# Kernel tuning notes

Hardware: AMD Instinct MI355X
Metric: run time of the kernel (lower is better)

## Reference

```python
import jax, jax.numpy as jnp
import numpy as np

N = 16383        # complete binary tree, 14 levels
D_NODE = 512
D_SSM = 512
D_STATE = 16
MAX_DEPTH = 14   # number of BFS levels (depth 0..13)
LN_EPS = 1e-5


def setup_inputs() -> dict:
    key = jax.random.key(0)
    ks = jax.random.split(key, 8)
    # tree structure: parent[i] = (i-1)//2, root has parent -1; BFS order == index order
    parent = np.concatenate([np.array([-1]), (np.arange(1, N) - 1) // 2]).astype(np.int64)
    depth = np.floor(np.log2(np.arange(N) + 1)).astype(np.int32)
    s = jax.random.normal(ks[0], (N, D_NODE), jnp.float32)
    w = jax.random.uniform(ks[1], (N,), jnp.float32, minval=0.01, maxval=1.0)
    # parameters (xavier-ish scales)
    W_in = jax.random.normal(ks[2], (D_SSM, D_NODE + 1), jnp.float32) * (1.0 / np.sqrt(D_NODE + 1))
    b_in = jnp.zeros((D_SSM,), jnp.float32)
    W_delta = jax.random.normal(ks[3], (D_SSM, D_SSM), jnp.float32) * (1.0 / np.sqrt(D_SSM))
    # dt-style bias init: softplus(b) ~ dt in [1e-3, 1e-1]
    dt = jnp.exp(jax.random.uniform(ks[4], (D_SSM,), jnp.float32) * (np.log(0.1) - np.log(0.001)) + np.log(0.001))
    b_delta = dt + jnp.log(-jnp.expm1(-dt))
    W_w = jax.random.normal(ks[5], (D_SSM, 1), jnp.float32)
    b_w = jnp.zeros((D_SSM,), jnp.float32)
    A_log = jnp.log(jnp.broadcast_to(jnp.arange(1.0, D_STATE + 1.0, dtype=jnp.float32)[None, :], (D_SSM, D_STATE)))
    D = jnp.ones((D_SSM,), jnp.float32)
    W_B = jax.random.normal(ks[6], (D_STATE, D_SSM), jnp.float32) * (1.0 / np.sqrt(D_SSM))
    b_B = jnp.zeros((D_STATE,), jnp.float32)
    W_C = jax.random.normal(ks[7], (D_STATE, D_SSM), jnp.float32) * (1.0 / np.sqrt(D_SSM))
    b_C = jnp.zeros((D_STATE,), jnp.float32)
    gamma = jnp.ones((D_SSM,), jnp.float32)
    beta = jnp.zeros((D_SSM,), jnp.float32)
    return {"s": s, "w": w, "parent": jnp.asarray(parent), "depth": jnp.asarray(depth),
            "W_in": W_in, "b_in": b_in, "W_delta": W_delta, "b_delta": b_delta,
            "W_w": W_w, "b_w": b_w, "A_log": A_log, "D": D,
            "W_B": W_B, "b_B": b_B, "W_C": W_C, "b_C": b_C,
            "gamma": gamma, "beta": beta}


def reference(s, w, parent, depth, W_in, b_in, W_delta, b_delta, W_w, b_w,
              A_log, D, W_B, b_B, W_C, b_C, gamma, beta):
    n = s.shape[0]
    log_w = jnp.log(w + 1e-6)[:, None]                       # [N, 1]
    feat = jnp.concatenate([s, log_w], axis=1)               # [N, d_node+1]
    x = feat @ W_in.T + b_in                                 # [N, d_ssm]
    delta = jax.nn.softplus(x @ W_delta.T + b_delta) * jax.nn.sigmoid(log_w @ W_w.T + b_w)  # [N, d_ssm]
    A = -jnp.exp(A_log)                                      # [d_ssm, d_state]
    B = x @ W_B.T + b_B                                      # [N, d_state]
    C = x @ W_C.T + b_C                                      # [N, d_state]
    A_bar = jnp.exp(delta[:, :, None] * A[None])             # [N, d_ssm, d_state]
    Bx = (delta * x)[:, :, None] * B[:, None, :]             # [N, d_ssm, d_state]
    # level-parallel tree scan: all nodes at BFS depth l updated together
    par = jnp.maximum(parent, 0)
    has_par = (parent >= 0)[:, None, None]
    H = jnp.zeros((n, A_bar.shape[1], A_bar.shape[2]), x.dtype)
    for lvl in range(MAX_DEPTH):
        h_par = jnp.where(has_par, jnp.take(H, par, axis=0), 0.0)
        H = jnp.where((depth == lvl)[:, None, None], A_bar * h_par + Bx, H)
    Y = jnp.einsum('nds,ns->nd', H, C) + D * x               # [N, d_ssm]
    mu = jnp.mean(Y, axis=-1, keepdims=True)
    var = jnp.var(Y, axis=-1, keepdims=True)
    return (Y - mu) / jnp.sqrt(var + LN_EPS) * gamma + beta
```

## Files before the change

kernel.cpp:

```cpp
#include <hip/hip_runtime.h>
#include <hip/hip_bf16.h>
#include <math.h>

#define D_SSM 512
#define D_STATE 16
#define CKPT_BASE 511
#define N_CKPT 512
#define MPAD 16384

typedef __attribute__((ext_vector_type(8))) short short8;
typedef __attribute__((ext_vector_type(4))) float floatx4;

__device__ __forceinline__ unsigned short f2bf(float f) {
    unsigned int u = __float_as_uint(f);
    unsigned int r = (u + 0x7fffu + ((u >> 16) & 1u)) >> 16;
    return (unsigned short)r;
}
__device__ __forceinline__ float bf2f(unsigned short u) {
    return __uint_as_float(((unsigned int)u) << 16);
}
__device__ __forceinline__ void g2lds16(const void* g, void* l) {
    __builtin_amdgcn_global_load_lds(
        (const __attribute__((address_space(1))) void*)g,
        (__attribute__((address_space(3))) void*)l, 16, 0, 0);
}

__device__ __forceinline__ void pw_powers(float r, float* p) {
    float r2 = r * r, r4 = r2 * r2, r8 = r4 * r4;
    p[0] = r;          p[1] = r2;         p[2] = r2 * r;     p[3] = r4;
    p[4] = r4 * r;     p[5] = r4 * r2;    p[6] = r4 * p[2];  p[7] = r8;
    p[8] = r8 * r;     p[9] = r8 * r2;    p[10] = r8 * p[2]; p[11] = r8 * r4;
    p[12] = r8 * p[4]; p[13] = r8 * p[5]; p[14] = r8 * p[6]; p[15] = r8 * r8;
}

__global__ __launch_bounds__(256) void prep_kernel(
    const float* __restrict__ s, const float* __restrict__ w,
    const float* __restrict__ W_in, const float* __restrict__ W_delta,
    const float* __restrict__ W_B, const float* __restrict__ W_C,
    unsigned short* __restrict__ s_bf, float* __restrict__ lw,
    unsigned short* __restrict__ Win_bf, unsigned short* __restrict__ Wd_bf,
    int Nn)
{
    const int b = blockIdx.x, t = threadIdx.x;
    if (b < MPAD) {
        unsigned int pack = 0;
        if (b < Nn) {
            float2 sv = *(const float2*)(s + (size_t)b * 512 + t * 2);
            pack = (unsigned int)f2bf(sv.x) | ((unsigned int)f2bf(sv.y) << 16);
        }
        *(unsigned int*)(s_bf + (size_t)b * 512 + t * 2) = pack;
        if (t == 0) lw[b] = (b < Nn) ? logf(w[b] + 1e-6f) : 0.f;
    } else if (b < MPAD + 512) {
        int c = b - MPAD;
        float a0 = W_in[(size_t)c * 513 + t * 2];
        float a1 = W_in[(size_t)c * 513 + t * 2 + 1];
        *(unsigned int*)(Win_bf + (size_t)c * 512 + t * 2) =
            (unsigned int)f2bf(a0) | ((unsigned int)f2bf(a1) << 16);
    } else if (b < MPAD + 1024) {
        int c = b - MPAD - 512;
        float2 wv = *(const float2*)(W_delta + (size_t)c * 512 + t * 2);
        *(unsigned int*)(Wd_bf + (size_t)c * 512 + t * 2) =
            (unsigned int)f2bf(wv.x) | ((unsigned int)f2bf(wv.y) << 16);
    } else {
        int c = b - MPAD - 1024;
        float2 wv; wv.x = 0.f; wv.y = 0.f;
        if (c < 16)      wv = *(const float2*)(W_B + (size_t)c * 512 + t * 2);
        else if (c < 32) wv = *(const float2*)(W_C + (size_t)(c - 16) * 512 + t * 2);
        *(unsigned int*)(Wd_bf + (size_t)(512 + c) * 512 + t * 2) =
            (unsigned int)f2bf(wv.x) | ((unsigned int)f2bf(wv.y) << 16);
    }
}

__global__ __launch_bounds__(256) void gemm_mfma(
    const unsigned short* __restrict__ Abf,
    const unsigned short* __restrict__ Wbf,
    float* __restrict__ outf,
    unsigned short* __restrict__ outbf,
    const float* __restrict__ bias,
    const float* __restrict__ lw,
    const float* __restrict__ wcol, int wcol_stride,
    const float* __restrict__ bw,
    const float* __restrict__ b_B, const float* __restrict__ b_C,
    float* __restrict__ Bm, float* __restrict__ Cm,
    int mode)
{
    __shared__ __align__(16) short As[2][128 * 32];
    __shared__ __align__(16) short Bs[2][128 * 32];
    const int tid = threadIdx.x;
    const int wave = tid >> 6, lane = tid & 63;

    const int nwg  = gridDim.x * gridDim.y;
    const int orig = blockIdx.y * gridDim.x + blockIdx.x;
    const int wsw  = (orig & 7) * (nwg >> 3) + (orig >> 3);
    const int bx   = wsw % gridDim.x;
    const int by   = wsw / gridDim.x;
    const int row0 = by * 128;
    const int col0 = bx * 128;

    const int wr = (wave >> 1) * 64;
    const int wc = (wave & 1) * 64;

    floatx4 acc[4][4] = {};

    const int srow = lane >> 2;
    const int sg   = (lane & 3) ^ ((srow >> 1) & 3);
    const int scol = sg * 8;

    const unsigned short* Ag = Abf + (size_t)(row0 + wave * 16 + srow) * 512 + scol;
    const unsigned short* Wg = Wbf + (size_t)(col0 + wave * 16 + srow) * 512 + scol;
    char* Al = (char*)&As[0][0] + wave * 1024;
    char* Bl = (char*)&Bs[0][0] + wave * 1024;

    #define STAGE(buf, k0)                                              \
        do {                                                            \
            g2lds16(Ag + (k0),            Al + (buf) * 8192);           \
            g2lds16(Ag + 64 * 512 + (k0), Al + (buf) * 8192 + 4096);    \
            g2lds16(Wg + (k0),            Bl + (buf) * 8192);           \
            g2lds16(Wg + 64 * 512 + (k0), Bl + (buf) * 8192 + 4096);    \
        } while (0)

    STAGE(0, 0);
    __syncthreads();

    for (int it = 0; it < 16; ++it) {
        const int cur = it & 1;
        if (it < 15) STAGE(cur ^ 1, (it + 1) * 32);

        short8 af[4], bfr[4];
        #pragma unroll
        for (int i = 0; i < 4; i++) {
            int m = wr + i * 16 + (lane & 15);
            int gm = (lane >> 4) ^ ((m >> 1) & 3);
            af[i] = *(const short8*)&As[cur][m * 32 + gm * 8];
        }
        #pragma unroll
        for (int j = 0; j < 4; j++) {
            int n = wc + j * 16 + (lane & 15);
            int gn = (lane >> 4) ^ ((n >> 1) & 3);
            bfr[j] = *(const short8*)&Bs[cur][n * 32 + gn * 8];
        }
        #pragma unroll
        for (int i = 0; i < 4; i++)
            #pragma unroll
            for (int j = 0; j < 4; j++)
                acc[i][j] = __builtin_amdgcn_mfma_f32_16x16x32_bf16(af[i], bfr[j], acc[i][j], 0, 0, 0);
        __syncthreads();
    }
    #undef STAGE

    if (col0 >= 512) {
        #pragma unroll
        for (int i = 0; i < 4; i++) {
            #pragma unroll
            for (int reg = 0; reg < 4; reg++) {
                int r = row0 + wr + i * 16 + (lane >> 4) * 4 + reg;
                #pragma unroll
                for (int j = 0; j < 4; j++) {
                    int c2 = wc + j * 16 + (lane & 15);
                    float z = acc[i][j][reg];
                    if (c2 < 16)      Bm[(size_t)r * 16 + c2]        = z + b_B[c2];
                    else if (c2 < 32) Cm[(size_t)r * 16 + (c2 - 16)] = z + b_C[c2 - 16];
                }
            }
        }
        return;
    }

    #pragma unroll
    for (int i = 0; i < 4; i++) {
        #pragma unroll
        for (int reg = 0; reg < 4; reg++) {
            int r = row0 + wr + i * 16 + (lane >> 4) * 4 + reg;
            float lwr = lw[r];
            #pragma unroll
            for (int j = 0; j < 4; j++) {
                int c = col0 + wc + j * 16 + (lane & 15);
                float z = acc[i][j][reg] + bias[c];
                if (mode == 0) {
                    float o = z + lwr * wcol[(size_t)c * wcol_stride];
                    outbf[(size_t)r * 512 + c] = f2bf(o);
                } else {
                    float sp = (z > 15.f) ? z : __logf(1.f + __expf(z));
                    float sg2 = __builtin_amdgcn_rcpf(1.f + __expf(-(lwr * wcol[c] + bw[c])));
                    outf[(size_t)r * 512 + c] = sp * sg2;
                }
            }
        }
    }
}

__global__ __launch_bounds__(512) void scan_shallow(
    const unsigned short* __restrict__ x_bf, const float* __restrict__ delta,
    const float* __restrict__ Bm, const float* __restrict__ Cm,
    const float* __restrict__ A_log, const float* __restrict__ Dv,
    const float* __restrict__ gamma, const float* __restrict__ beta,
    float* __restrict__ out)
{
    __shared__ __align__(16) float Banc[9][16];
    __shared__ __align__(16) float Cn[16];
    __shared__ float red[16];
    const int n = blockIdx.x;
    const int d = threadIdx.x;

    if (d < 144) {
        int k = d >> 4, s = d & 15;
        int a = n;
        for (int q = 0; q < 9; q++) if (q < k) a = (a < 0) ? -1 : ((a - 1) >> 1);
        Banc[k][s] = (a >= 0) ? Bm[(size_t)a * 16 + s] : 0.f;
    }
    if (d >= 240 && d < 256) Cn[d - 240] = Cm[(size_t)n * 16 + (d - 240)];
    __syncthreads();

    float As0 = -__expf(A_log[d * 16]);
    bool fast = true;
    #pragma unroll
    for (int s = 1; s < 16; s++) {
        float As = -__expf(A_log[d * 16 + s]);
        fast = fast && (fabsf(As - (float)(s + 1) * As0) <= 1e-4f * (float)(s + 1));
    }

    float acc[16];
    #pragma unroll
    for (int s = 0; s < 16; s++) acc[s] = 0.f;

    float cum = 0.f;
    int a = n;
    #pragma unroll
    for (int k = 0; k < 9; k++) {
        if (a >= 0) {
            float da = delta[(size_t)a * 512 + d];
            float bx = da * bf2f(x_bf[(size_t)a * 512 + d]);
            if (fast) {
                float r = __expf(As0 * cum);
                float pw[16]; pw_powers(r, pw);
                const floatx4* B4 = (const floatx4*)&Banc[k][0];
                #pragma unroll
                for (int q = 0; q < 4; q++) {
                    floatx4 b = B4[q];
                    #pragma unroll
                    for (int u = 0; u < 4; u++) {
                        int s = q * 4 + u;
                        acc[s] = fmaf(bx * pw[s], b[u], acc[s]);
                    }
                }
            } else {
                #pragma unroll
                for (int s = 0; s < 16; s++) {
                    float As = -__expf(A_log[d * 16 + s]);
                    acc[s] = fmaf(bx * __expf(As * cum), Banc[k][s], acc[s]);
                }
            }
            cum += da;
            a = (a - 1) >> 1;
        }
    }

    float xv = bf2f(x_bf[(size_t)n * 512 + d]);
    float y0 = 0.f, y1 = 0.f;
    const floatx4* C4 = (const floatx4*)&Cn[0];
    #pragma unroll
    for (int q = 0; q < 4; q++) {
        floatx4 c = C4[q];
        #pragma unroll
        for (int u = 0; u < 4; u++) {
            int s = q * 4 + u;
            if (s & 1) y1 = fmaf(c[u], acc[s], y1);
            else       y0 = fmaf(c[u], acc[s], y0);
        }
    }
    float y = fmaf(Dv[d], xv, y0 + y1);

    float s1 = y, s2 = y * y;
    #pragma unroll
    for (int off = 32; off > 0; off >>= 1) {
        s1 += __shfl_xor(s1, off);
        s2 += __shfl_xor(s2, off);
    }
    int wid = d >> 6, lane = d & 63;
    if (lane == 0) { red[wid] = s1; red[wid + 8] = s2; }
    __syncthreads();
    float S1 = 0.f, S2 = 0.f;
    #pragma unroll
    for (int k = 0; k < 8; k++) { S1 += red[k]; S2 += red[k + 8]; }
    float mu = S1 * (1.f / 512.f);
    float var = S2 * (1.f / 512.f) - mu * mu;
    float inv = rsqrtf(var + 1e-5f);
    out[(size_t)n * 512 + d] = (y - mu) * inv * gamma[d] + beta[d];
}

__global__ __launch_bounds__(512) void scan_deep(
    const unsigned short* __restrict__ x_bf, const float* __restrict__ delta,
    const float* __restrict__ Bm, const float* __restrict__ Cm,
    const float* __restrict__ A_log, const float* __restrict__ Dv,
    const float* __restrict__ gamma, const float* __restrict__ beta,
    float* __restrict__ out)
{
    __shared__ float Y[16][512];
    __shared__ __align__(16) float BCs[31][32];
    __shared__ __align__(16) float Banc[10][16];
    __shared__ int nid[16];
    const int p = blockIdx.x;
    const int d = threadIdx.x;
    const int a9 = CKPT_BASE + p;

    for (int idx = d; idx < 31 * 32; idx += 512) {
        int i = idx >> 5, c = idx & 31;
        int v = i + 1;
        int j = 31 - __builtin_clz((unsigned)v);
        int node = ((a9 + 1) << j) - 1 + (v - (1 << j));
        BCs[i][c] = (c < 16) ? Bm[(size_t)node * 16 + c] : Cm[(size_t)node * 16 + (c - 16)];
    }
    if (d < 160) {
        int k = d >> 4, s = d & 15;
        int a = a9;
        for (int q = 0; q < k; q++) a = (a - 1) >> 1;
        Banc[k][s] = Bm[(size_t)a * 16 + s];
    }
    __syncthreads();

    float As0 = -__expf(A_log[d * 16]);
    bool fast = true;
    #pragma unroll
    for (int s = 1; s < 16; s++) {
        float As = -__expf(A_log[d * 16 + s]);
        fast = fast && (fabsf(As - (float)(s + 1) * As0) <= 1e-4f * (float)(s + 1));
    }
    const float dvd = Dv[d];

    float H9v[16];
    #pragma unroll
    for (int s = 0; s < 16; s++) H9v[s] = 0.f;
    {
        float cum = 0.f;
        int a = a9;
        #pragma unroll
        for (int k = 0; k < 10; k++) {
            float da = delta[(size_t)a * 512 + d];
            float bx = da * bf2f(x_bf[(size_t)a * 512 + d]);
            if (fast) {
                float r = __expf(As0 * cum);
                float pw[16]; pw_powers(r, pw);
                const floatx4* B4 = (const floatx4*)&Banc[k][0];
                #pragma unroll
                for (int q = 0; q < 4; q++) {
                    floatx4 b = B4[q];
                    #pragma unroll
                    for (int u = 0; u < 4; u++) {
                        int s = q * 4 + u;
                        H9v[s] = fmaf(bx * pw[s], b[u], H9v[s]);
                    }
                }
            } else {
                #pragma unroll
                for (int s = 0; s < 16; s++) {
                    float As = -__expf(A_log[d * 16 + s]);
                    H9v[s] = fmaf(bx * __expf(As * cum), Banc[k][s], H9v[s]);
                }
            }
            cum += da;
            a = (a - 1) >> 1;
        }
    }

    auto step = [&](int n, int bfs, const float* Hp, float* Hc, int slot) {
        float dlt = delta[(size_t)n * 512 + d];
        float xv = bf2f(x_bf[(size_t)n * 512 + d]);
        float bx = dlt * xv;
        const floatx4* B4 = (const floatx4*)&BCs[bfs][0];
        const floatx4* C4 = (const floatx4*)&BCs[bfs][16];
        float y0 = 0.f, y1 = 0.f;
        if (fast) {
            float r = __expf(As0 * dlt);
            float pw[16]; pw_powers(r, pw);
            #pragma unroll
            for (int q = 0; q < 4; q++) {
                floatx4 b = B4[q], c = C4[q];
                #pragma unroll
                for (int u = 0; u < 4; u++) {
                    int s = q * 4 + u;
                    Hc[s] = fmaf(pw[s], Hp[s], bx * b[u]);
                    if (s & 1) y1 = fmaf(c[u], Hc[s], y1);
                    else       y0 = fmaf(c[u], Hc[s], y0);
                }
            }
        } else {
            #pragma unroll
            for (int s = 0; s < 16; s++) {
                float Ab = __expf(dlt * (-__expf(A_log[d * 16 + s])));
                Hc[s] = fmaf(Ab, Hp[s], bx * BCs[bfs][s]);
                float cc = BCs[bfs][16 + s];
                if (s & 1) y1 = fmaf(cc, Hc[s], y1);
                else       y0 = fmaf(cc, Hc[s], y0);
            }
        }
        Y[slot][d] = fmaf(dvd, xv, y0 + y1);
        if (d == 0) nid[slot] = n;
    };

    auto flush = [&](int cnt) {
        const int w = d >> 6, lane = d & 63;
        for (int i = w; i < cnt; i += 8) {
            int n = nid[i];
            float v[8]; float s1 = 0.f, s2 = 0.f;
            #pragma unroll
            for (int k = 0; k < 8; k++) {
                v[k] = Y[i][lane + 64 * k];
                s1 += v[k]; s2 += v[k] * v[k];
            }
            #pragma unroll
            for (int off = 32; off > 0; off >>= 1) {
                s1 += __shfl_xor(s1, off);
                s2 += __shfl_xor(s2, off);
            }
            float mu = s1 * (1.f / 512.f);
            float inv = rsqrtf(s2 * (1.f / 512.f) - mu * mu + 1e-5f);
            #pragma unroll
            for (int k = 0; k < 8; k++) {
                int ch = lane + 64 * k;
                out[(size_t)n * 512 + ch] = (v[k] - mu) * inv * gamma[ch] + beta[ch];
            }
        }
    };

    float H10[16], H11[16], H12[16], H13[16];
    #pragma unroll
    for (int c0 = 0; c0 < 2; c0++) {
        int slot = 0;
        if (c0 == 0) {
            float xv = bf2f(x_bf[(size_t)a9 * 512 + d]);
            const floatx4* C4 = (const floatx4*)&BCs[0][16];
            float y0 = 0.f, y1 = 0.f;
            #pragma unroll
            for (int q = 0; q < 4; q++) {
                floatx4 c = C4[q];
                #pragma unroll
                for (int u = 0; u < 4; u++) {
                    int s = q * 4 + u;
                    if (s & 1) y1 = fmaf(c[u], H9v[s], y1);
                    else       y0 = fmaf(c[u], H9v[s], y0);
                }
            }
            Y[0][d] = fmaf(dvd, xv, y0 + y1);
            if (d == 0) nid[0] = a9;
            slot = 1;
        }
        int n10 = 2 * a9 + 1 + c0;
        step(n10, 1 + c0, H9v, H10, slot++);
        #pragma unroll
        for (int c1 = 0; c1 < 2; c1++) {
            int n11 = 2 * n10 + 1 + c1;
            step(n11, 3 + 2 * c0 + c1, H10, H11, slot++);
            #pragma unroll
            for (int c2 = 0; c2 < 2; c2++) {
                int n12 = 2 * n11 + 1 + c2;
                step(n12, 7 + 4 * c0 + 2 * c1 + c2, H11, H12, slot++);
                #pragma unroll
                for (int c3 = 0; c3 < 2; c3++) {
                    int n13 = 2 * n12 + 1 + c3;
                    step(n13, 15 + 8 * c0 + 4 * c1 + 2 * c2 + c3, H12, H13, slot++);
                }
            }
        }
        __syncthreads();
        flush(c0 == 0 ? 16 : 15);
        __syncthreads();
    }
}

extern "C" void kernel_launch(void* const* d_in, const int* in_sizes, int n_in,
                              void* d_out, int out_size, void* d_ws, size_t ws_size,
                              hipStream_t stream) {
    const float* s_in   = (const float*)d_in[0];
    const float* w      = (const float*)d_in[1];
    const float* W_in    = (const float*)d_in[4];
    const float* b_in    = (const float*)d_in[5];
    const float* W_delta = (const float*)d_in[6];
    const float* b_delta = (const float*)d_in[7];
    const float* W_w     = (const float*)d_in[8];
    const float* b_w     = (const float*)d_in[9];
    const float* A_log   = (const float*)d_in[10];
    const float* Dv      = (const float*)d_in[11];
    const float* W_B     = (const float*)d_in[12];
    const float* b_B     = (const float*)d_in[13];
    const float* W_C     = (const float*)d_in[14];
    const float* b_C     = (const float*)d_in[15];
    const float* gamma   = (const float*)d_in[16];
    const float* beta    = (const float*)d_in[17];
    float* out = (float*)d_out;

    const int Nn = in_sizes[1];

    float* ws    = (float*)d_ws;
    float* lw    = ws;
    float* delta = lw + MPAD;
    float* Bm    = delta + (size_t)MPAD * 512;
    float* Cm    = Bm + (size_t)MPAD * 16;
    unsigned short* s_bf  = (unsigned short*)(Cm + (size_t)MPAD * 16);
    unsigned short* x_bf  = s_bf + (size_t)MPAD * 512;
    unsigned short* Win_bf = x_bf + (size_t)MPAD * 512;
    unsigned short* Wd_bf  = Win_bf + 512 * 512;

    prep_kernel<<<MPAD + 1024 + 128, 256, 0, stream>>>(s_in, w, W_in, W_delta, W_B, W_C,
                                                       s_bf, lw, Win_bf, Wd_bf, Nn);

    dim3 g1(4, 128);
    gemm_mfma<<<g1, 256, 0, stream>>>(s_bf, Win_bf, nullptr, x_bf,
                                      b_in, lw, W_in + 512, 513, nullptr,
                                      nullptr, nullptr, nullptr, nullptr, 0);
    dim3 g2(5, 128);
    gemm_mfma<<<g2, 256, 0, stream>>>(x_bf, Wd_bf, delta, nullptr,
                                      b_delta, lw, W_w, 1, b_w,
                                      b_B, b_C, Bm, Cm, 1);

    scan_shallow<<<CKPT_BASE, 512, 0, stream>>>(x_bf, delta, Bm, Cm, A_log, Dv,
                                                gamma, beta, out);

    scan_deep<<<N_CKPT, 512, 0, stream>>>(x_bf, delta, Bm, Cm, A_log, Dv,
                                          gamma, beta, out);
}
```

Baseline: 222.2 us.

## Fuse shallow and deep scan kernels with prefetching and precomputed A tables

Merges the shallow-node and deep-subtree scan kernels into one launch. Deep blocks take the first block indices and shallow blocks fill in behind them. The per-channel A_log exp and fast-path check move into the prep kernel as small tables. The deep path now software-prefetches ancestor and subtree delta/x values into registers ahead of use, and leaf nodes skip storing state. This removes a launch and hides global-load latency, at the cost of more registers, with launch bounds set to 4 blocks per CU.

Result: slower. 234.1 us (+5.3%).

```diff
diff --git a/kernel.cpp b/kernel.cpp
--- a/kernel.cpp
+++ b/kernel.cpp
@@ -37,8 +37,10 @@
     const float* __restrict__ s, const float* __restrict__ w,
     const float* __restrict__ W_in, const float* __restrict__ W_delta,
     const float* __restrict__ W_B, const float* __restrict__ W_C,
+    const float* __restrict__ A_log,
     unsigned short* __restrict__ s_bf, float* __restrict__ lw,
     unsigned short* __restrict__ Win_bf, unsigned short* __restrict__ Wd_bf,
+    float* __restrict__ As_tab, int* __restrict__ fast_tab,
     int Nn)
 {
     const int b = blockIdx.x, t = threadIdx.x;
@@ -61,13 +63,24 @@
         float2 wv = *(const float2*)(W_delta + (size_t)c * 512 + t * 2);
         *(unsigned int*)(Wd_bf + (size_t)c * 512 + t * 2) =
             (unsigned int)f2bf(wv.x) | ((unsigned int)f2bf(wv.y) << 16);
-    } else {
+    } else if (b < MPAD + 1024 + 128) {
         int c = b - MPAD - 1024;
         float2 wv; wv.x = 0.f; wv.y = 0.f;
         if (c < 16)      wv = *(const float2*)(W_B + (size_t)c * 512 + t * 2);
         else if (c < 32) wv = *(const float2*)(W_C + (size_t)(c - 16) * 512 + t * 2);
         *(unsigned int*)(Wd_bf + (size_t)(512 + c) * 512 + t * 2) =
             (unsigned int)f2bf(wv.x) | ((unsigned int)f2bf(wv.y) << 16);
+    } else {
+        int ch = (b - (MPAD + 1024 + 128)) * 256 + t;
+        float As0 = -__expf(A_log[ch * 16]);
+        bool ok = true;
+        #pragma unroll
+        for (int q = 1; q < 16; q++) {
+            float As = -__expf(A_log[ch * 16 + q]);
+            ok = ok && (fabsf(As - (float)(q + 1) * As0) <= 1e-4f * (float)(q + 1));
+        }
+        As_tab[ch] = As0;
+        fast_tab[ch] = ok ? 1 : 0;
     }
 }
 
@@ -189,281 +202,351 @@
     }
 }
 
-__global__ __launch_bounds__(512) void scan_shallow(
+__global__ __launch_bounds__(512, 4) void scan_fused(
     const unsigned short* __restrict__ x_bf, const float* __restrict__ delta,
     const float* __restrict__ Bm, const float* __restrict__ Cm,
     const float* __restrict__ A_log, const float* __restrict__ Dv,
     const float* __restrict__ gamma, const float* __restrict__ beta,
+    const float* __restrict__ As_tab, const int* __restrict__ fast_tab,
     float* __restrict__ out)
 {
-    __shared__ __align__(16) float Banc[9][16];
-    __shared__ __align__(16) float Cn[16];
-    __shared__ float red[16];
-    const int n = blockIdx.x;
+    __shared__ __align__(16) float SMEM[16 * 512 + 31 * 32 + 10 * 16];
+    __shared__ int nid[16];
+    const int bid = blockIdx.x;
     const int d = threadIdx.x;
 
-    if (d < 144) {
-        int k = d >> 4, s = d & 15;
-        int a = n;
-        for (int q = 0; q < 9; q++) if (q < k) a = (a < 0) ? -1 : ((a - 1) >> 1);
-        Banc[k][s] = (a >= 0) ? Bm[(size_t)a * 16 + s] : 0.f;
-    }
-    if (d >= 240 && d < 256) Cn[d - 240] = Cm[(size_t)n * 16 + (d - 240)];
-    __syncthreads();
-
-    float As0 = -__expf(A_log[d * 16]);
-    bool fast = true;
-    #pragma unroll
-    for (int s = 1; s < 16; s++) {
-        float As = -__expf(A_log[d * 16 + s]);
-        fast = fast && (fabsf(As - (float)(s + 1) * As0) <= 1e-4f * (float)(s + 1));
-    }
-
-    float acc[16];
-    #pragma unroll
-    for (int s = 0; s < 16; s++) acc[s] = 0.f;
-
-    float cum = 0.f;
-    int a = n;
-    #pragma unroll
-    for (int k = 0; k < 9; k++) {
-        if (a >= 0) {
-            float da = delta[(size_t)a * 512 + d];
-            float bx = da * bf2f(x_bf[(size_t)a * 512 + d]);
+    const float As0 = As_tab[d];
+    const bool fast = fast_tab[d] != 0;
+    const float dvd = Dv[d];
+
+    if (bid < N_CKPT) {
+        const int a9 = CKPT_BASE + bid;
+        float* const Yb   = SMEM;
+        float* const BCs  = SMEM + 8192;
+        float* const Banc = SMEM + 8192 + 992;
+
+        for (int idx = d; idx < 31 * 32; idx += 512) {
+            int i = idx >> 5, c = idx & 31;
+            int v = i + 1;
+            int j = 31 - __builtin_clz((unsigned)v);
+            int node = ((a9 + 1) << j) - 1 + (v - (1 << j));
+            BCs[i * 32 + c] = (c < 16) ? Bm[(size_t)node * 16 + c]
+                                       : Cm[(size_t)node * 16 + (c - 16)];
+        }
+        if (d < 160) {
+            int k = d >> 4, ss = d & 15;
+            int a = a9;
+            for (int q = 0; q < k; q++) a = (a - 1) >> 1;
+            Banc[k * 16 + ss] = Bm[(size_t)a * 16 + ss];
+        }
+
+        float adl[10]; unsigned short axr[10];
+        {
+            int a = a9;
+            #pragma unroll
+            for (int k = 0; k < 10; k++) {
+                adl[k] = delta[(size_t)a * 512 + d];
+                axr[k] = x_bf[(size_t)a * 512 + d];
+                a = (a - 1) >> 1;
+            }
+        }
+
+        const int n10a = 2 * a9 + 1, n10b = 2 * a9 + 2;
+        float pdl[2][7]; unsigned short pxr[2][7]; int pid[2][7];
+        auto pf7 = [&](int n11, float* dl, unsigned short* xr, int* id) {
+            id[0] = n11;          id[1] = 2 * n11 + 1; id[2] = 2 * id[1] + 1;
+            id[3] = id[2] + 1;    id[4] = 2 * n11 + 2; id[5] = 2 * id[4] + 1;
+            id[6] = id[5] + 1;
+            #pragma unroll
+            for (int q = 0; q < 7; q++) {
+                dl[q] = delta[(size_t)id[q] * 512 + d];
+                xr[q] = x_bf[(size_t)id[q] * 512 + d];
+            }
+        };
+        float d10a = delta[(size_t)n10a * 512 + d];
+        unsigned short x10a = x_bf[(size_t)n10a * 512 + d];
+        pf7(2 * n10a + 1, pdl[0], pxr[0], pid[0]);
+
+        __syncthreads();
+
+        float H9v[16];
+        #pragma unroll
+        for (int ss = 0; ss < 16; ss++) H9v[ss] = 0.f;
+        {
+            float cum = 0.f;
+            #pragma unroll
+            for (int k = 0; k < 10; k++) {
+                float da = adl[k];
+                float bx = da * bf2f(axr[k]);
+                if (fast) {
+                    float r = __expf(As0 * cum);
+                    float pw[16]; pw_powers(r, pw);
+                    const floatx4* B4 = (const floatx4*)&Banc[k * 16];
+                    #pragma unroll
+                    for (int q = 0; q < 4; q++) {
+                        floatx4 b = B4[q];
+                        #pragma unroll
+                        for (int u = 0; u < 4; u++) {
+                            int ss = q * 4 + u;
+                            H9v[ss] = fmaf(bx * pw[ss], b[u], H9v[ss]);
+                        }
+                    }
+                } else {
+                    #pragma unroll
+                    for (int ss = 0; ss < 16; ss++) {
+                        float As = -__expf(A_log[d * 16 + ss]);
+                        H9v[ss] = fmaf(bx * __expf(As * cum), Banc[k * 16 + ss], H9v[ss]);
+                    }
+                }
+                cum += da;
+            }
+        }
+
+        auto step_pf = [&](int bfs, float dlt, unsigned short xraw,
+                           const float* Hp, float* Hc, int slot, int n) {
+            float xv = bf2f(xraw);
+            float bx = dlt * xv;
+            float y0 = 0.f, y1 = 0.f;
+            const floatx4* B4 = (const floatx4*)&BCs[bfs * 32];
+            const floatx4* C4 = (const floatx4*)&BCs[bfs * 32 + 16];
+            if (fast) {
+                float r = __expf(As0 * dlt);
+                float pw[16]; pw_powers(r, pw);
+                #pragma unroll
+                for (int q = 0; q < 4; q++) {
+                    floatx4 b = B4[q], c = C4[q];
+                    #pragma unroll
+                    for (int u = 0; u < 4; u++) {
+                        int ss = q * 4 + u;
+                        Hc[ss] = fmaf(pw[ss], Hp[ss], bx * b[u]);
+                        if (ss & 1) y1 = fmaf(c[u], Hc[ss], y1);
+                        else        y0 = fmaf(c[u], Hc[ss], y0);
+                    }
+                }
+            } else {
+                #pragma unroll
+                for (int ss = 0; ss < 16; ss++) {
+                    float Ab = __expf(dlt * (-__expf(A_log[d * 16 + ss])));
+                    Hc[ss] = fmaf(Ab, Hp[ss], bx * BCs[bfs * 32 + ss]);
+                    float cc = BCs[bfs * 32 + 16 + ss];
+                    if (ss & 1) y1 = fmaf(cc, Hc[ss], y1);
+                    else        y0 = fmaf(cc, Hc[ss], y0);
+                }
+            }
+            Yb[slot * 512 + d] = fmaf(dvd, xv, y0 + y1);
+            if (d == 0) nid[slot] = n;
+        };
+        auto leaf_pf = [&](int bfs, float dlt, unsigned short xraw,
+                           const float* Hp, int slot, int n) {
+            float xv = bf2f(xraw);
+            float bx = dlt * xv;
+            float y0 = 0.f, y1 = 0.f;
+            const floatx4* B4 = (const floatx4*)&BCs[bfs * 32];
+            const floatx4* C4 = (const floatx4*)&BCs[bfs * 32 + 16];
+            if (fast) {
+                float r = __expf(As0 * dlt);
+                float pw[16]; pw_powers(r, pw);
+                #pragma unroll
+                for (int q = 0; q < 4; q++) {
+                    floatx4 b = B4[q], c = C4[q];
+                    #pragma unroll
+                    for (int u = 0; u < 4; u++) {
+                        int ss = q * 4 + u;
+                        float h = fmaf(pw[ss], Hp[ss], bx * b[u]);
+                        if (ss & 1) y1 = fmaf(c[u], h, y1);
+                        else        y0 = fmaf(c[u], h, y0);
+                    }
+                }
+            } else {
+                #pragma unroll
+                for (int ss = 0; ss < 16; ss++) {
+                    float Ab = __expf(dlt * (-__expf(A_log[d * 16 + ss])));
+                    float h = fmaf(Ab, Hp[ss], bx * BCs[bfs * 32 + ss]);
+                    float cc = BCs[bfs * 32 + 16 + ss];
+                    if (ss & 1) y1 = fmaf(cc, h, y1);
+                    else        y0 = fmaf(cc, h, y0);
+                }
+            }
+            Yb[slot * 512 + d] = fmaf(dvd, xv, y0 + y1);
+            if (d == 0) nid[slot] = n;
+        };
+        auto flush = [&](int cnt) {
+            const int w = d >> 6, lane = d & 63;
+            for (int i = w; i < cnt; i += 8) {
+                int n = nid[i];
+                float v[8]; float s1 = 0.f, s2 = 0.f;
+                #pragma unroll
+                for (int k = 0; k < 8; k++) {
+                    v[k] = Yb[i * 512 + lane + 64 * k];
+                    s1 += v[k]; s2 += v[k] * v[k];
+                }
+                #pragma unroll
+                for (int off = 32; off > 0; off >>= 1) {
+                    s1 += __shfl_xor(s1, off);
+                    s2 += __shfl_xor(s2, off);
+                }
+                float mu = s1 * (1.f / 512.f);
+                float inv = rsqrtf(s2 * (1.f / 512.f) - mu * mu + 1e-5f);
+                #pragma unroll
+                for (int k = 0; k < 8; k++) {
+                    int ch = lane + 64 * k;
+                    out[(size_t)n * 512 + ch] = (v[k] - mu) * inv * gamma[ch] + beta[ch];
+                }
+            }
+        };
+
+        {
+            float xv = bf2f(axr[0]);
+            const floatx4* C4 = (const floatx4*)&BCs[16];
+            float y0 = 0.f, y1 = 0.f;
+            #pragma unroll
+            for (int q = 0; q < 4; q++) {
+                floatx4 c = C4[q];
+                #pragma unroll
+                for (int u = 0; u < 4; u++) {
+                    int ss = q * 4 + u;
+                    if (ss & 1) y1 = fmaf(c[u], H9v[ss], y1);
+                    else        y0 = fmaf(c[u], H9v[ss], y0);
+                }
+            }
+            Yb[d] = fmaf(dvd, xv, y0 + y1);
+            if (d == 0) nid[0] = a9;
+        }
+
+        float H10[16], H11[16], H12[16];
+        float d10b; unsigned short x10b;
+
+        step_pf(1, d10a, x10a, H9v, H10, 1, n10a);
+        pf7(2 * n10a + 2, pdl[1], pxr[1], pid[1]);
+        step_pf(3,  pdl[0][0], pxr[0][0], H10, H11, 2, pid[0][0]);
+        step_pf(7,  pdl[0][1], pxr[0][1], H11, H12, 3, pid[0][1]);
+        leaf_pf(15, pdl[0][2], pxr[0][2], H12, 4, pid[0][2]);
+        leaf_pf(16, pdl[0][3], pxr[0][3], H12, 5, pid[0][3]);
+        step_pf(8,  pdl[0][4], pxr[0][4], H11, H12, 6, pid[0][4]);
+        leaf_pf(17, pdl[0][5], pxr[0][5], H12, 7, pid[0][5]);
+        leaf_pf(18, pdl[0][6], pxr[0][6], H12, 8, pid[0][6]);
+        d10b = delta[(size_t)n10b * 512 + d];
+        x10b = x_bf[(size_t)n10b * 512 + d];
+        pf7(2 * n10b + 1, pdl[0], pxr[0], pid[0]);
+        step_pf(4,  pdl[1][0], pxr[1][0], H10, H11, 9,  pid[1][0]);
+        step_pf(9,  pdl[1][1], pxr[1][1], H11, H12, 10, pid[1][1]);
+        leaf_pf(19, pdl[1][2], pxr[1][2], H12, 11, pid[1][2]);
+        leaf_pf(20, pdl[1][3], pxr[1][3], H12, 12, pid[1][3]);
+        step_pf(10, pdl[1][4], pxr[1][4], H11, H12, 13, pid[1][4]);
+        leaf_pf(21, pdl[1][5], pxr[1][5], H12, 14, pid[1][5]);
+        leaf_pf(22, pdl[1][6], pxr[1][6], H12, 15, pid[1][6]);
+        __syncthreads();
+        flush(16);
+        __syncthreads();
+
+        step_pf(2, d10b, x10b, H9v, H10, 0, n10b);
+        pf7(2 * n10b + 2, pdl[1], pxr[1], pid[1]);
+        step_pf(5,  pdl[0][0], pxr[0][0], H10, H11, 1, pid[0][0]);
+        step_pf(11, pdl[0][1], pxr[0][1], H11, H12, 2, pid[0][1]);
+        leaf_pf(23, pdl[0][2], pxr[0][2], H12, 3, pid[0][2]);
+        leaf_pf(24, pdl[0][3], pxr[0][3], H12, 4, pid[0][3]);
+        step_pf(12, pdl[0][4], pxr[0][4], H11, H12, 5, pid[0][4]);
+        leaf_pf(25, pdl[0][5], pxr[0][5], H12, 6, pid[0][5]);
+        leaf_pf(26, pdl[0][6], pxr[0][6], H12, 7, pid[0][6]);
+        step_pf(6,  pdl[1][0], pxr[1][0], H10, H11, 8,  pid[1][0]);
+        step_pf(13, pdl[1][1], pxr[1][1], H11, H12, 9,  pid[1][1]);
+        leaf_pf(27, pdl[1][2], pxr[1][2], H12, 10, pid[1][2]);
+        leaf_pf(28, pdl[1][3], pxr[1][3], H12, 11, pid[1][3]);
+        step_pf(14, pdl[1][4], pxr[1][4], H11, H12, 12, pid[1][4]);
+        leaf_pf(29, pdl[1][5], pxr[1][5], H12, 13, pid[1][5]);
+        leaf_pf(30, pdl[1][6], pxr[1][6], H12, 14, pid[1][6]);
+        __syncthreads();
+        flush(15);
+    } else {
+        const int n = bid - N_CKPT;
+        float* const Banc9 = SMEM;
+        float* const Cn    = SMEM + 144;
+        float* const red   = SMEM + 160;
+
+        if (d < 144) {
+            int k = d >> 4, ss = d & 15;
+            int a = n;
+            for (int q = 0; q < 9; q++) if (q < k) a = (a < 0) ? -1 : ((a - 1) >> 1);
+            Banc9[k * 16 + ss] = (a >= 0) ? Bm[(size_t)a * 16 + ss] : 0.f;
+        }
+        if (d >= 240 && d < 256) Cn[d - 240] = Cm[(size_t)n * 16 + (d - 240)];
+
+        float adl[9]; unsigned short axr[9];
+        {
+            int a = n;
+            #pragma unroll
+            for (int k = 0; k < 9; k++) {
+                bool v = a >= 0;
+                adl[k] = v ? delta[(size_t)a * 512 + d] : 0.f;
+                axr[k] = v ? x_bf[(size_t)a * 512 + d] : (unsigned short)0;
+                a = v ? ((a - 1) >> 1) : -1;
+            }
+        }
+        __syncthreads();
+
+        float acc[16];
+        #pragma unroll
+        for (int ss = 0; ss < 16; ss++) acc[ss] = 0.f;
+
+        float cum = 0.f;
+        #pragma unroll
+        for (int k = 0; k < 9; k++) {
+            float da = adl[k];
+            float bx = da * bf2f(axr[k]);
             if (fast) {
                 float r = __expf(As0 * cum);
                 float pw[16]; pw_powers(r, pw);
-                const floatx4* B4 = (const floatx4*)&Banc[k][0];
+                const floatx4* B4 = (const floatx4*)&Banc9[k * 16];
                 #pragma unroll
                 for (int q = 0; q < 4; q++) {
                     floatx4 b = B4[q];
                     #pragma unroll
                     for (int u = 0; u < 4; u++) {
-                        int s = q * 4 + u;
-                        acc[s] = fmaf(bx * pw[s], b[u], acc[s]);
+                        int ss = q * 4 + u;
+                        acc[ss] = fmaf(bx * pw[ss], b[u], acc[ss]);
                     }
                 }
             } else {
                 #pragma unroll
-                for (int s = 0; s < 16; s++) {
-                    float As = -__expf(A_log[d * 16 + s]);
-                    acc[s] = fmaf(bx * __expf(As * cum), Banc[k][s], acc[s]);
+                for (int ss = 0; ss < 16; ss++) {
+                    float As = -__expf(A_log[d * 16 + ss]);
+                    acc[ss] = fmaf(bx * __expf(As * cum), Banc9[k * 16 + ss], acc[ss]);
                 }
             }
             cum += da;
-            a = (a - 1) >> 1;
-        }
-    }
-
-    float xv = bf2f(x_bf[(size_t)n * 512 + d]);
-    float y0 = 0.f, y1 = 0.f;
-    const floatx4* C4 = (const floatx4*)&Cn[0];
-    #pragma unroll
-    for (int q = 0; q < 4; q++) {
-        floatx4 c = C4[q];
-        #pragma unroll
-        for (int u = 0; u < 4; u++) {
-            int s = q * 4 + u;
-            if (s & 1) y1 = fmaf(c[u], acc[s], y1);
-            else       y0 = fmaf(c[u], acc[s], y0);
-        }
-    }
-    float y = fmaf(Dv[d], xv, y0 + y1);
-
-    float s1 = y, s2 = y * y;
-    #pragma unroll
-    for (int off = 32; off > 0; off >>= 1) {
-        s1 += __shfl_xor(s1, off);
-        s2 += __shfl_xor(s2, off);
-    }
-    int wid = d >> 6, lane = d & 63;
-    if (lane == 0) { red[wid] = s1; red[wid + 8] = s2; }
-    __syncthreads();
-    float S1 = 0.f, S2 = 0.f;
-    #pragma unroll
-    for (int k = 0; k < 8; k++) { S1 += red[k]; S2 += red[k + 8]; }
-    float mu = S1 * (1.f / 512.f);
-    float var = S2 * (1.f / 512.f) - mu * mu;
-    float inv = rsqrtf(var + 1e-5f);
-    out[(size_t)n * 512 + d] = (y - mu) * inv * gamma[d] + beta[d];
-}
-
-__global__ __launch_bounds__(512) void scan_deep(
-    const unsigned short* __restrict__ x_bf, const float* __restrict__ delta,
-    const float* __restrict__ Bm, const float* __restrict__ Cm,
-    const float* __restrict__ A_log, const float* __restrict__ Dv,
-    const float* __restrict__ gamma, const float* __restrict__ beta,
-    float* __restrict__ out)
-{
-    __shared__ float Y[16][512];
-    __shared__ __align__(16) float BCs[31][32];
-    __shared__ __align__(16) float Banc[10][16];
-    __shared__ int nid[16];
-    const int p = blockIdx.x;
-    const int d = threadIdx.x;
-    const int a9 = CKPT_BASE + p;
-
-    for (int idx = d; idx < 31 * 32; idx += 512) {
-        int i = idx >> 5, c = idx & 31;
-        int v = i + 1;
-        int j = 31 - __builtin_clz((unsigned)v);
-        int node = ((a9 + 1) << j) - 1 + (v - (1 << j));
-        BCs[i][c] = (c < 16) ? Bm[(size_t)node * 16 + c] : Cm[(size_t)node * 16 + (c - 16)];
-    }
-    if (d < 160) {
-        int k = d >> 4, s = d & 15;
-        int a = a9;
-        for (int q = 0; q < k; q++) a = (a - 1) >> 1;
-        Banc[k][s] = Bm[(size_t)a * 16 + s];
-    }
-    __syncthreads();
-
-    float As0 = -__expf(A_log[d * 16]);
-    bool fast = true;
-    #pragma unroll
-    for (int s = 1; s < 16; s++) {
-        float As = -__expf(A_log[d * 16 + s]);
-        fast = fast && (fabsf(As - (float)(s + 1) * As0) <= 1e-4f * (float)(s + 1));
-    }
-    const float dvd = Dv[d];
-
-    float H9v[16];
-    #pragma unroll
-    for (int s = 0; s < 16; s++) H9v[s] = 0.f;
-    {
-        float cum = 0.f;
-        int a = a9;
-        #pragma unroll
-        for (int k = 0; k < 10; k++) {
-            float da = delta[(size_t)a * 512 + d];
-            float bx = da * bf2f(x_bf[(size_t)a * 512 + d]);
-            if (fast) {
-                float r = __expf(As0 * cum);
-                float pw[16]; pw_powers(r, pw);
-                const floatx4* B4 = (const floatx4*)&Banc[k][0];
-                #pragma unroll
-                for (int q = 0; q < 4; q++) {
-                    floatx4 b = B4[q];
-                    #pragma unroll
-                    for (int u = 0; u < 4; u++) {
-                        int s = q * 4 + u;
-                        H9v[s] = fmaf(bx * pw[s], b[u], H9v[s]);
-                    }
-                }
-            } else {
-                #pragma unroll
-                for (int s = 0; s < 16; s++) {
-                    float As = -__expf(A_log[d * 16 + s]);
-                    H9v[s] = fmaf(bx * __expf(As * cum), Banc[k][s], H9v[s]);
-                }
-            }
-            cum += da;
-            a = (a - 1) >> 1;
-        }
-    }
-
-    auto step = [&](int n, int bfs, const float* Hp, float* Hc, int slot) {
-        float dlt = delta[(size_t)n * 512 + d];
-        float xv = bf2f(x_bf[(size_t)n * 512 + d]);
-        float bx = dlt * xv;
-        const floatx4* B4 = (const floatx4*)&BCs[bfs][0];
-        const floatx4* C4 = (const floatx4*)&BCs[bfs][16];
+        }
+
+        float xv = bf2f(axr[0]);
         float y0 = 0.f, y1 = 0.f;
-        if (fast) {
-            float r = __expf(As0 * dlt);
-            float pw[16]; pw_powers(r, pw);
-            #pragma unroll
-            for (int q = 0; q < 4; q++) {
-                floatx4 b = B4[q], c = C4[q];
-                #pragma unroll
-                for (int u = 0; u < 4; u++) {
-                    int s = q * 4 + u;
-                    Hc[s] = fmaf(pw[s], Hp[s], bx * b[u]);
-                    if (s & 1) y1 = fmaf(c[u], Hc[s], y1);
-                    else       y0 = fmaf(c[u], Hc[s], y0);
-                }
-            }
-        } else {
-            #pragma unroll
-            for (int s = 0; s < 16; s++) {
-                float Ab = __expf(dlt * (-__expf(A_log[d * 16 + s])));
-                Hc[s] = fmaf(Ab, Hp[s], bx * BCs[bfs][s]);
-                float cc = BCs[bfs][16 + s];
-                if (s & 1) y1 = fmaf(cc, Hc[s], y1);
-                else       y0 = fmaf(cc, Hc[s], y0);
-            }
-        }
-        Y[slot][d] = fmaf(dvd, xv, y0 + y1);
-        if (d == 0) nid[slot] = n;
-    };
-
-    auto flush = [&](int cnt) {
-        const int w = d >> 6, lane = d & 63;
-        for (int i = w; i < cnt; i += 8) {
-            int n = nid[i];
-            float v[8]; float s1 = 0.f, s2 = 0.f;
-            #pragma unroll
-            for (int k = 0; k < 8; k++) {
-                v[k] = Y[i][lane + 64 * k];
-                s1 += v[k]; s2 += v[k] * v[k];
-            }
-            #pragma unroll
-            for (int off = 32; off > 0; off >>= 1) {
-                s1 += __shfl_xor(s1, off);
-                s2 += __shfl_xor(s2, off);
-            }
-            float mu = s1 * (1.f / 512.f);
-            float inv = rsqrtf(s2 * (1.f / 512.f) - mu * mu + 1e-5f);
-            #pragma unroll
-            for (int k = 0; k < 8; k++) {
-                int ch = lane + 64 * k;
-                out[(size_t)n * 512 + ch] = (v[k] - mu) * inv * gamma[ch] + beta[ch];
-            }
-        }
-    };
-
-    float H10[16], H11[16], H12[16], H13[16];
-    #pragma unroll
-    for (int c0 = 0; c0 < 2; c0++) {
-        int slot = 0;
-        if (c0 == 0) {
-            float xv = bf2f(x_bf[(size_t)a9 * 512 + d]);
-            const floatx4* C4 = (const floatx4*)&BCs[0][16];
-            float y0 = 0.f, y1 = 0.f;
-            #pragma unroll
-            for (int q = 0; q < 4; q++) {
-                floatx4 c = C4[q];
-                #pragma unroll
-                for (int u = 0; u < 4; u++) {
-                    int s = q * 4 + u;
-                    if (s & 1) y1 = fmaf(c[u], H9v[s], y1);
-                    else       y0 = fmaf(c[u], H9v[s], y0);
-                }
-            }
-            Y[0][d] = fmaf(dvd, xv, y0 + y1);
-            if (d == 0) nid[0] = a9;
-            slot = 1;
-        }
-        int n10 = 2 * a9 + 1 + c0;
-        step(n10, 1 + c0, H9v, H10, slot++);
-        #pragma unroll
-        for (int c1 = 0; c1 < 2; c1++) {
-            int n11 = 2 * n10 + 1 + c1;
-            step(n11, 3 + 2 * c0 + c1, H10, H11, slot++);
-            #pragma unroll
-            for (int c2 = 0; c2 < 2; c2++) {
-                int n12 = 2 * n11 + 1 + c2;
-                step(n12, 7 + 4 * c0 + 2 * c1 + c2, H11, H12, slot++);
-                #pragma unroll
-                for (int c3 = 0; c3 < 2; c3++) {
-                    int n13 = 2 * n12 + 1 + c3;
-                    step(n13, 15 + 8 * c0 + 4 * c1 + 2 * c2 + c3, H12, H13, slot++);
-                }
-            }
-        }
+        const floatx4* C4 = (const floatx4*)&Cn[0];
+        #pragma unroll
+        for (int q = 0; q < 4; q++) {
+            floatx4 c = C4[q];
+            #pragma unroll
+            for (int u = 0; u < 4; u++) {
+                int ss = q * 4 + u;
+                if (ss & 1) y1 = fmaf(c[u], acc[ss], y1);
+                else        y0 = fmaf(c[u], acc[ss], y0);
+            }
+        }
+        float y = fmaf(dvd, xv, y0 + y1);
+
+        float s1 = y, s2 = y * y;
+        #pragma unroll
+        for (int off = 32; off > 0; off >>= 1) {
+            s1 += __shfl_xor(s1, off);
+            s2 += __shfl_xor(s2, off);
+        }
+        int wid = d >> 6, lane = d & 63;
+        if (lane == 0) { red[wid] = s1; red[wid + 8] = s2; }
         __syncthreads();
-        flush(c0 == 0 ? 16 : 15);
-        __syncthreads();
+        float S1 = 0.f, S2 = 0.f;
+        #pragma unroll
+        for (int k = 0; k < 8; k++) { S1 += red[k]; S2 += red[k + 8]; }
+        float mu = S1 * (1.f / 512.f);
+        float var = S2 * (1.f / 512.f) - mu * mu;
+        float inv = rsqrtf(var + 1e-5f);
+        out[(size_t)n * 512 + d] = (y - mu) * inv * gamma[d] + beta[d];
     }
 }
 
@@ -499,9 +582,12 @@
     unsigned short* x_bf  = s_bf + (size_t)MPAD * 512;
     unsigned short* Win_bf = x_bf + (size_t)MPAD * 512;
     unsigned short* Wd_bf  = Win_bf + 512 * 512;
-
-    prep_kernel<<<MPAD + 1024 + 128, 256, 0, stream>>>(s_in, w, W_in, W_delta, W_B, W_C,
-                                                       s_bf, lw, Win_bf, Wd_bf, Nn);
+    float* As_tab  = (float*)(Wd_bf + 640 * 512);
+    int*   fast_tab = (int*)(As_tab + 512);
+
+    prep_kernel<<<MPAD + 1024 + 128 + 2, 256, 0, stream>>>(
+        s_in, w, W_in, W_delta, W_B, W_C, A_log,
+        s_bf, lw, Win_bf, Wd_bf, As_tab, fast_tab, Nn);
 
     dim3 g1(4, 128);
     gemm_mfma<<<g1, 256, 0, stream>>>(s_bf, Win_bf, nullptr, x_bf,
@@ -512,9 +598,6 @@
                                       b_delta, lw, W_w, 1, b_w,
                                       b_B, b_C, Bm, Cm, 1);
 
-    scan_shallow<<<CKPT_BASE, 512, 0, stream>>>(x_bf, delta, Bm, Cm, A_log, Dv,
-                                                gamma, beta, out);
-
-    scan_deep<<<N_CKPT, 512, 0, stream>>>(x_bf, delta, Bm, Cm, A_log, Dv,
-                                          gamma, beta, out);
-}
+    scan_fused<<<N_CKPT + CKPT_BASE, 512, 0, stream>>>(
+        x_bf, delta, Bm, Cm, A_log, Dv, gamma, beta, As_tab, fast_tab, out);
+}
```
